# Optimization experiments

Measured on AMD Instinct MI355X. Metric: run time of the kernel, lower is better.

Reference implementation:

```python
import jax, jax.numpy as jnp
import numpy as np

B, D, N, H = 16384, 8, 64, 128   # batch, input_path_dim, cde_state_dim, vf_hidden_dim
NSIG = D + D * (D - 1) // 2       # Lyndon words up to depth 2: letters + pairs i<j


def setup_inputs() -> dict:
    key = jax.random.key(0)
    ks = jax.random.split(key, 6)
    g = lambda k, shape, scale: jax.random.normal(k, shape, jnp.float32) * scale
    return {
        "h": jax.random.normal(ks[0], (B, N), jnp.float32),
        "primitive_signature": jax.random.normal(ks[1], (B, NSIG), jnp.float32) * 0.1,
        "W1": g(ks[2], (H, N), (1.0 / N) ** 0.5),
        "b1": jnp.zeros((H,), jnp.float32),
        "W2": g(ks[3], (H, H), (1.0 / H) ** 0.5),
        "b2": jnp.zeros((H,), jnp.float32),
        "W3": g(ks[4], (D * N, H), (1.0 / H) ** 0.5),
        "b3": jnp.zeros((D * N,), jnp.float32),
    }


def reference(h, primitive_signature, W1, b1, W2, b2, W3, b3):
    d, n = D, N
    iu, ju = np.triu_indices(d, k=1)  # level-2 Lyndon words ij with i<j, lex order

    def vf(hv):  # MLP vector field: (n,) -> (d, n), one field per input channel
        z = jax.nn.softplus(W1 @ hv + b1)
        z = jax.nn.softplus(W2 @ z + b2)
        return jnp.tanh(W3 @ z + b3).reshape(d, n)

    def single(hv, sig):
        V = vf(hv)  # (d, n) level-1 brackets (the vector fields themselves)
        # JVP of the whole stacked field in direction t: J_{V_j}(h) @ t for all j
        jvp_dir = lambda t: jax.jvp(vf, (hv,), (t,))[1]  # (d, n)
        JV = jax.vmap(jvp_dir)(V)                         # (i, j, n) = J_{V_j} V_i
        # Lie bracket [V_i, V_j](h) = J_{V_j} V_i - J_{V_i} V_j
        br2 = JV - jnp.swapaxes(JV, 0, 1)                 # (i, j, n)
        lyn2 = br2[iu, ju]                                # (d*(d-1)/2, n)
        # log-ODE contraction: sum_w logsig_w * bracket_w(h)
        return sig[:d] @ V + sig[d:] @ lyn2               # (n,)

    return jax.vmap(single)(h, primitive_signature)
```

## Files before the change

### kernel.cpp

```cpp
#include <hip/hip_runtime.h>
#include <hip/hip_bf16.h>

#define NEL 16384

#define W1B_OFF 0
#define W2B_OFF 8192
#define W3B_OFF 24576
#define WS_WEIGHTS 90112
#define S1_OFF  90112
#define S2_OFF  (S1_OFF + NEL*128)
#define V_OFF   (S2_OFF + NEL*128)
#define DZ2_OFF (V_OFF + NEL*512)

typedef __attribute__((ext_vector_type(8))) short bf16x8;
typedef __attribute__((ext_vector_type(4))) float f32x4;

__device__ __forceinline__ float bf2f(unsigned int u16) {
    unsigned int x = u16 << 16;
    float f; __builtin_memcpy(&f, &x, 4); return f;
}
__device__ __forceinline__ unsigned short f2bf(float f) {
    unsigned int x; __builtin_memcpy(&x, &f, 4);
    x = (x + 0x7FFFu + ((x >> 16) & 1u)) >> 16;
    return (unsigned short)x;
}
__device__ __forceinline__ void unpack8(uint4 q, float* f) {
    f[0] = bf2f(q.x & 0xFFFFu); f[1] = bf2f(q.x >> 16);
    f[2] = bf2f(q.y & 0xFFFFu); f[3] = bf2f(q.y >> 16);
    f[4] = bf2f(q.z & 0xFFFFu); f[5] = bf2f(q.z >> 16);
    f[6] = bf2f(q.w & 0xFFFFu); f[7] = bf2f(q.w >> 16);
}
__device__ __forceinline__ void sp_sig(float x, float& sp, float& sig) {
    float t = __expf(-fabsf(x));
    float r = __builtin_amdgcn_rcpf(1.f + t);
    sig = (x >= 0.f) ? r : 1.f - r;
    sp  = fmaxf(x, 0.f) + __logf(1.f + t);
}
__device__ __forceinline__ float tanh_fast(float x) {
    float t = __expf(-2.f * fabsf(x));
    float y = (1.f - t) * __builtin_amdgcn_rcpf(1.f + t);
    unsigned int xb, yb;
    __builtin_memcpy(&xb, &x, 4);
    __builtin_memcpy(&yb, &y, 4);
    yb |= (xb & 0x80000000u);
    float rr; __builtin_memcpy(&rr, &yb, 4);
    return rr;
}
__device__ __forceinline__ bf16x8 ldfrag(const unsigned short* p) {
    return *reinterpret_cast<const bf16x8*>(p);
}
__device__ __forceinline__ void cpu4(unsigned short* dst, const unsigned short* src) {
    *reinterpret_cast<uint4*>(dst) = *reinterpret_cast<const uint4*>(src);
}

__global__ void prep_weights(const float* __restrict__ W1,
                             const float* __restrict__ W2,
                             const float* __restrict__ W3,
                             unsigned short* __restrict__ wb) {
    int i = blockIdx.x * blockDim.x + threadIdx.x;
    if (i >= WS_WEIGHTS) return;
    float v;
    if (i < W2B_OFF) v = W1[i];
    else if (i < W3B_OFF) v = W2[i - W2B_OFF];
    else v = W3[i - W3B_OFF];
    wb[i] = f2bf(v);
}

#define K12_LDS 39168
__global__ __launch_bounds__(256, 4)
void k12_fwd(const float* __restrict__ hg,
             const float* __restrict__ b1,
             const float* __restrict__ b2,
             const float* __restrict__ b3,
             unsigned short* __restrict__ wsb) {
    __shared__ __align__(16) char sm[K12_LDS];
    unsigned short* w1s = (unsigned short*)(sm);
    unsigned short* hs  = (unsigned short*)(sm + 18432);
    unsigned short* w2s = (unsigned short*)(sm);
    unsigned short* wc  = (unsigned short*)(sm);
    unsigned short* z1s = (unsigned short*)(sm + 34816);
    unsigned short* z2s = (unsigned short*)(sm + 34816);
    unsigned short* S1g = wsb + S1_OFF;
    unsigned short* S2g = wsb + S2_OFF;
    unsigned short* Vg  = wsb + V_OFF;

    const int tid = threadIdx.x;
    const int e0 = blockIdx.x * 16;
    const int lane = tid & 63;
    const int w = tid >> 6;
    const int r16 = lane & 15;
    const int kb = lane >> 4;
    const int crow = kb * 4;

    #pragma unroll
    for (int q = 0; q < 4; ++q) {
        int idx = q * 256 + tid;
        int row = idx >> 3, u4 = idx & 7;
        cpu4(&w1s[row * 72 + u4 * 8], &wsb[W1B_OFF + row * 64 + u4 * 8]);
    }
    {
        int row = tid >> 4, f4 = tid & 15;
        float4 hv = *reinterpret_cast<const float4*>(&hg[(e0 + row) * 64 + f4 * 4]);
        ushort2 lo = { f2bf(hv.x), f2bf(hv.y) };
        ushort2 hi = { f2bf(hv.z), f2bf(hv.w) };
        *reinterpret_cast<ushort2*>(&hs[row * 72 + f4 * 4]) = lo;
        *reinterpret_cast<ushort2*>(&hs[row * 72 + f4 * 4 + 2]) = hi;
    }
    __syncthreads();

    {
        const unsigned short* Ab = hs + r16 * 72 + kb * 8;
        bf16x8 a0 = ldfrag(Ab), a1 = ldfrag(Ab + 32);
        f32x4 acc[2] = {};
        #pragma unroll
        for (int t = 0; t < 2; ++t) {
            int col16 = (w * 2 + t) * 16 + r16;
            const unsigned short* Bb = w1s + col16 * 72 + kb * 8;
            acc[t] = __builtin_amdgcn_mfma_f32_16x16x32_bf16(a0, ldfrag(Bb), acc[t], 0, 0, 0);
            acc[t] = __builtin_amdgcn_mfma_f32_16x16x32_bf16(a1, ldfrag(Bb + 32), acc[t], 0, 0, 0);
        }
        #pragma unroll
        for (int t = 0; t < 2; ++t) {
            int col = (w * 2 + t) * 16 + r16;
            float bb = b1[col];
            #pragma unroll
            for (int rr = 0; rr < 4; ++rr) {
                int e = crow + rr;
                float sp, sg;
                sp_sig(acc[t][rr] + bb, sp, sg);
                z1s[e * 136 + col] = f2bf(sp);
                S1g[(e0 + e) * 128 + col] = f2bf(sg);
            }
        }
    }
    __syncthreads();

    #pragma unroll
    for (int q = 0; q < 8; ++q) {
        int idx = q * 256 + tid;
        int row = idx >> 4, u4 = idx & 15;
        cpu4(&w2s[row * 136 + u4 * 8], &wsb[W2B_OFF + row * 128 + u4 * 8]);
    }
    __syncthreads();

    {
        const unsigned short* Ab = z1s + r16 * 136 + kb * 8;
        bf16x8 a[4];
        #pragma unroll
        for (int ks = 0; ks < 4; ++ks) a[ks] = ldfrag(Ab + ks * 32);
        __syncthreads();
        f32x4 acc[2] = {};
        #pragma unroll
        for (int t = 0; t < 2; ++t) {
            int col16 = (w * 2 + t) * 16 + r16;
            const unsigned short* Bb = w2s + col16 * 136 + kb * 8;
            #pragma unroll
            for (int ks = 0; ks < 4; ++ks)
                acc[t] = __builtin_amdgcn_mfma_f32_16x16x32_bf16(a[ks], ldfrag(Bb + ks * 32), acc[t], 0, 0, 0);
        }
        #pragma unroll
        for (int t = 0; t < 2; ++t) {
            int col = (w * 2 + t) * 16 + r16;
            float bb = b2[col];
            #pragma unroll
            for (int rr = 0; rr < 4; ++rr) {
                int e = crow + rr;
                float sp, sg;
                sp_sig(acc[t][rr] + bb, sp, sg);
                z2s[e * 136 + col] = f2bf(sp);
                S2g[(e0 + e) * 128 + col] = f2bf(sg);
            }
        }
    }

    for (int nc = 0; nc < 4; ++nc) {
        __syncthreads();
        #pragma unroll
        for (int q = 0; q < 8; ++q) {
            int idx = q * 256 + tid;
            int row = idx >> 4, u4 = idx & 15;
            cpu4(&wc[row * 136 + u4 * 8], &wsb[W3B_OFF + (nc * 128 + row) * 128 + u4 * 8]);
        }
        __syncthreads();

        const unsigned short* Ab = z2s + r16 * 136 + kb * 8;
        bf16x8 a[4];
        #pragma unroll
        for (int ks = 0; ks < 4; ++ks) a[ks] = ldfrag(Ab + ks * 32);
        f32x4 acc[2] = {};
        #pragma unroll
        for (int t = 0; t < 2; ++t) {
            int col16 = (w * 2 + t) * 16 + r16;
            const unsigned short* Bb = wc + col16 * 136 + kb * 8;
            #pragma unroll
            for (int ks = 0; ks < 4; ++ks)
                acc[t] = __builtin_amdgcn_mfma_f32_16x16x32_bf16(a[ks], ldfrag(Bb + ks * 32), acc[t], 0, 0, 0);
        }
        #pragma unroll
        for (int t = 0; t < 2; ++t) {
            int c = nc * 128 + (w * 2 + t) * 16 + r16;
            float bb = b3[c];
            #pragma unroll
            for (int rr = 0; rr < 4; ++rr) {
                int e = crow + rr;
                float v = tanh_fast(acc[t][rr] + bb);
                Vg[(e0 + e) * 512 + c] = f2bf(v);
            }
        }
    }
}

#define K3_LDS 53376
__global__ __launch_bounds__(256, 3)
void k3_jvp12(const float* __restrict__ sigg,
              unsigned short* __restrict__ wsb) {
    __shared__ __align__(16) char sm[K3_LDS];
    unsigned short* vs   = (unsigned short*)(sm);
    unsigned short* w1s  = (unsigned short*)(sm + 8320);
    unsigned short* ts   = (unsigned short*)(sm + 26752);
    unsigned short* dz1s = (unsigned short*)(sm);
    unsigned short* w2s  = (unsigned short*)(sm + 17408);
    float* sigsm = (float*)(sm + 52224);
    const unsigned short* S1g = wsb + S1_OFF;
    const unsigned short* S2g = wsb + S2_OFF;
    const unsigned short* Vg  = wsb + V_OFF;
    unsigned short* DZ2g = wsb + DZ2_OFF;

    const int tid = threadIdx.x;
    const int e0 = blockIdx.x * 8;
    const int lane = tid & 63;
    const int w = tid >> 6;
    const int r16 = lane & 15;
    const int kb = lane >> 4;

    #pragma unroll
    for (int q = 0; q < 2; ++q) {
        int idx = q * 256 + tid;
        int row = idx >> 6, u4 = idx & 63;
        cpu4(&vs[row * 520 + u4 * 8], &Vg[(e0 + row) * 512 + u4 * 8]);
    }
    #pragma unroll
    for (int q = 0; q < 4; ++q) {
        int idx = q * 256 + tid;
        int row = idx >> 3, u4 = idx & 7;
        cpu4(&w1s[row * 72 + u4 * 8], &wsb[W1B_OFF + row * 64 + u4 * 8]);
    }
    #pragma unroll
    for (int q = 0; q < 2; ++q) {
        int idx = q * 256 + tid;
        if (idx < 288) sigsm[idx] = sigg[e0 * 36 + idx];
    }
    __syncthreads();

    {
        int m = tid >> 2, kq = tid & 3;
        int e = m >> 3, j = m & 7;
        float c8[8];
        #pragma unroll
        for (int i = 0; i < 8; ++i) {
            float v = 0.f;
            if (i < j) {
                int p = 7 * i - i * (i - 1) / 2 + (j - i - 1);
                v = sigsm[e * 36 + 8 + p];
            } else if (i > j) {
                int p = 7 * j - j * (j - 1) / 2 + (i - j - 1);
                v = -sigsm[e * 36 + 8 + p];
            }
            c8[i] = v;
        }
        float acc[16] = {};
        #pragma unroll
        for (int i = 0; i < 8; ++i) {
            uint4 qa = *reinterpret_cast<const uint4*>(&vs[e * 520 + i * 64 + kq * 16]);
            uint4 qb = *reinterpret_cast<const uint4*>(&vs[e * 520 + i * 64 + kq * 16 + 8]);
            float fa[8], fb[8];
            unpack8(qa, fa); unpack8(qb, fb);
            #pragma unroll
            for (int kk = 0; kk < 8; ++kk) {
                acc[kk]     += c8[i] * fa[kk];
                acc[kk + 8] += c8[i] * fb[kk];
            }
        }
        unsigned short o[16];
        #pragma unroll
        for (int kk = 0; kk < 16; ++kk) o[kk] = f2bf(acc[kk]);
        uint4 qo;
        qo.x = (unsigned int)o[0] | ((unsigned int)o[1] << 16);
        qo.y = (unsigned int)o[2] | ((unsigned int)o[3] << 16);
        qo.z = (unsigned int)o[4] | ((unsigned int)o[5] << 16);
        qo.w = (unsigned int)o[6] | ((unsigned int)o[7] << 16);
        *reinterpret_cast<uint4*>(&ts[m * 72 + kq * 16]) = qo;
        qo.x = (unsigned int)o[8]  | ((unsigned int)o[9]  << 16);
        qo.y = (unsigned int)o[10] | ((unsigned int)o[11] << 16);
        qo.z = (unsigned int)o[12] | ((unsigned int)o[13] << 16);
        qo.w = (unsigned int)o[14] | ((unsigned int)o[15] << 16);
        *reinterpret_cast<uint4*>(&ts[m * 72 + kq * 16 + 8]) = qo;
    }
    __syncthreads();

    float dz1v[8][4];
    const int rbase = w * 16 + kb * 4;
    const int e_loc = rbase >> 3;
    {
        const unsigned short* Ab = ts + (w * 16 + r16) * 72 + kb * 8;
        bf16x8 a0 = ldfrag(Ab), a1 = ldfrag(Ab + 32);
        f32x4 acc[8] = {};
        #pragma unroll
        for (int nt = 0; nt < 8; ++nt) {
            const unsigned short* Bb = w1s + (nt * 16 + r16) * 72 + kb * 8;
            acc[nt] = __builtin_amdgcn_mfma_f32_16x16x32_bf16(a0, ldfrag(Bb), acc[nt], 0, 0, 0);
            acc[nt] = __builtin_amdgcn_mfma_f32_16x16x32_bf16(a1, ldfrag(Bb + 32), acc[nt], 0, 0, 0);
        }
        #pragma unroll
        for (int nt = 0; nt < 8; ++nt) {
            int col = nt * 16 + r16;
            float s1v = bf2f(S1g[(e0 + e_loc) * 128 + col]);
            #pragma unroll
            for (int rr = 0; rr < 4; ++rr)
                dz1v[nt][rr] = acc[nt][rr] * s1v;
        }
    }
    __syncthreads();

    #pragma unroll
    for (int nt = 0; nt < 8; ++nt) {
        int col = nt * 16 + r16;
        #pragma unroll
        for (int rr = 0; rr < 4; ++rr)
            dz1s[(rbase + rr) * 136 + col] = f2bf(dz1v[nt][rr]);
    }
    #pragma unroll
    for (int q = 0; q < 8; ++q) {
        int idx = q * 256 + tid;
        int row = idx >> 4, u4 = idx & 15;
        cpu4(&w2s[row * 136 + u4 * 8], &wsb[W2B_OFF + row * 128 + u4 * 8]);
    }
    __syncthreads();

    {
        const unsigned short* Ab = dz1s + (w * 16 + r16) * 136 + kb * 8;
        bf16x8 a[4];
        #pragma unroll
        for (int ks = 0; ks < 4; ++ks) a[ks] = ldfrag(Ab + ks * 32);
        f32x4 acc[8] = {};
        #pragma unroll
        for (int nt = 0; nt < 8; ++nt) {
            const unsigned short* Bb = w2s + (nt * 16 + r16) * 136 + kb * 8;
            #pragma unroll
            for (int ks = 0; ks < 4; ++ks)
                acc[nt] = __builtin_amdgcn_mfma_f32_16x16x32_bf16(a[ks], ldfrag(Bb + ks * 32), acc[nt], 0, 0, 0);
        }
        #pragma unroll
        for (int nt = 0; nt < 8; ++nt) {
            int col = nt * 16 + r16;
            float s2v = bf2f(S2g[(e0 + e_loc) * 128 + col]);
            #pragma unroll
            for (int rr = 0; rr < 4; ++rr)
                DZ2g[(e0 * 8 + rbase + rr) * 128 + col] = f2bf(acc[nt][rr] * s2v);
        }
    }
}

#define K4_LDS 35392
__global__ __launch_bounds__(256, 4)
void k4_jvp3(const float* __restrict__ sigg,
             const unsigned short* __restrict__ wsb,
             float* __restrict__ out) {
    __shared__ __align__(16) char sm[K4_LDS];
    unsigned short* w3j0 = (unsigned short*)(sm);
    unsigned short* w3j1 = (unsigned short*)(sm + 17408);
    float*          sg1  = (float*)(sm + 34816);
    const unsigned short* Vg = wsb + V_OFF;
    const unsigned short* DZ2g = wsb + DZ2_OFF;

    const int tid = threadIdx.x;
    const int e0 = blockIdx.x * 16;
    const int lane = tid & 63;
    const int w = tid >> 6;
    const int r16 = lane & 15;
    const int kb = lane >> 4;
    const int crow = kb * 4;
    const int np = w * 16 + r16;

    if (tid < 128) {
        int e = tid >> 3, j7 = tid & 7;
        sg1[e * 9 + j7] = sigg[(e0 + e) * 36 + j7];
    }
    #pragma unroll
    for (int q = 0; q < 4; ++q) {
        int idx = q * 256 + tid;
        int row = idx >> 4, u4 = idx & 15;
        cpu4(&w3j0[row * 136 + u4 * 8], &wsb[W3B_OFF + row * 128 + u4 * 8]);
    }
    __syncthreads();

    float oacc[4] = {};
    const unsigned short* Agbase = DZ2g + (e0 + r16) * 8 * 128 + kb * 8;

    for (int j = 0; j < 8; ++j) {
        unsigned short* cur = (j & 1) ? w3j1 : w3j0;
        unsigned short* nxt = (j & 1) ? w3j0 : w3j1;
        if (j < 7) {
            #pragma unroll
            for (int q = 0; q < 4; ++q) {
                int idx = q * 256 + tid;
                int row = idx >> 4, u4 = idx & 15;
                cpu4(&nxt[row * 136 + u4 * 8], &wsb[W3B_OFF + ((j + 1) * 64 + row) * 128 + u4 * 8]);
            }
        }
        const unsigned short* Ag = Agbase + j * 128;
        bf16x8 a[4];
        #pragma unroll
        for (int ks = 0; ks < 4; ++ks) a[ks] = ldfrag(Ag + ks * 32);
        f32x4 acc = {};
        const unsigned short* Bb = cur + np * 136 + kb * 8;
        #pragma unroll
        for (int ks = 0; ks < 4; ++ks)
            acc = __builtin_amdgcn_mfma_f32_16x16x32_bf16(a[ks], ldfrag(Bb + ks * 32), acc, 0, 0, 0);

        #pragma unroll
        for (int rr = 0; rr < 4; ++rr) {
            int e = crow + rr;
            float v = bf2f(Vg[(e0 + e) * 512 + j * 64 + np]);
            float sv = sg1[e * 9 + j];
            oacc[rr] += sv * v + (1.f - v * v) * acc[rr];
        }
        __syncthreads();
    }

    #pragma unroll
    for (int rr = 0; rr < 4; ++rr)
        out[(e0 + crow + rr) * 64 + np] = oacc[rr];
}

extern "C" void kernel_launch(void* const* d_in, const int* in_sizes, int n_in,
                              void* d_out, int out_size, void* d_ws, size_t ws_size,
                              hipStream_t stream) {
    const float* hg  = (const float*)d_in[0];
    const float* sg  = (const float*)d_in[1];
    const float* W1  = (const float*)d_in[2];
    const float* b1  = (const float*)d_in[3];
    const float* W2  = (const float*)d_in[4];
    const float* b2  = (const float*)d_in[5];
    const float* W3  = (const float*)d_in[6];
    const float* b3  = (const float*)d_in[7];
    float* outp = (float*)d_out;
    unsigned short* wsb = (unsigned short*)d_ws;

    hipLaunchKernelGGL(prep_weights, dim3((WS_WEIGHTS + 255) / 256), dim3(256), 0, stream,
                       W1, W2, W3, wsb);
    hipLaunchKernelGGL(k12_fwd, dim3(NEL / 16), dim3(256), 0, stream, hg, b1, b2, b3, wsb);
    hipLaunchKernelGGL(k3_jvp12, dim3(NEL / 8), dim3(256), 0, stream, sg, wsb);
    hipLaunchKernelGGL(k4_jvp3, dim3(NEL / 16), dim3(256), 0, stream, sg, wsb, outp);
}
```

Baseline: 76.29 us.

## Read MFMA weight fragments directly from global memory instead of staging in LDS

In the forward kernel and the final JVP kernel, weight tiles are no longer copied into shared memory. Each lane loads its B fragments straight from global/L2, so the LDS copy loops and most block barriers go away, and shared memory per block shrinks sharply. The aim is to drop staging overhead and synchronisation and to raise occupancy. The cost is redundant global loads of the same weights across waves and blocks, plus uncoalesced row-strided fragment reads. Passing the workspace as separate const input and output pointers with __restrict__ is technically aliasing, since both point to the same buffer.

```diff
diff --git a/kernel.cpp b/kernel.cpp
--- a/kernel.cpp
+++ b/kernel.cpp
@@ -66,23 +66,21 @@
     wb[i] = f2bf(v);
 }
 
-#define K12_LDS 39168
+#define K12_LDS 11008
 __global__ __launch_bounds__(256, 4)
 void k12_fwd(const float* __restrict__ hg,
              const float* __restrict__ b1,
              const float* __restrict__ b2,
              const float* __restrict__ b3,
-             unsigned short* __restrict__ wsb) {
+             const unsigned short* __restrict__ wsb,
+             unsigned short* __restrict__ wso) {
     __shared__ __align__(16) char sm[K12_LDS];
-    unsigned short* w1s = (unsigned short*)(sm);
-    unsigned short* hs  = (unsigned short*)(sm + 18432);
-    unsigned short* w2s = (unsigned short*)(sm);
-    unsigned short* wc  = (unsigned short*)(sm);
-    unsigned short* z1s = (unsigned short*)(sm + 34816);
-    unsigned short* z2s = (unsigned short*)(sm + 34816);
-    unsigned short* S1g = wsb + S1_OFF;
-    unsigned short* S2g = wsb + S2_OFF;
-    unsigned short* Vg  = wsb + V_OFF;
+    unsigned short* hs  = (unsigned short*)(sm);
+    unsigned short* z1s = (unsigned short*)(sm + 2304);
+    unsigned short* z2s = (unsigned short*)(sm + 6656);
+    unsigned short* S1g = wso + S1_OFF;
+    unsigned short* S2g = wso + S2_OFF;
+    unsigned short* Vg  = wso + V_OFF;
 
     const int tid = threadIdx.x;
     const int e0 = blockIdx.x * 16;
@@ -92,12 +90,6 @@
     const int kb = lane >> 4;
     const int crow = kb * 4;
 
-    #pragma unroll
-    for (int q = 0; q < 4; ++q) {
-        int idx = q * 256 + tid;
-        int row = idx >> 3, u4 = idx & 7;
-        cpu4(&w1s[row * 72 + u4 * 8], &wsb[W1B_OFF + row * 64 + u4 * 8]);
-    }
     {
         int row = tid >> 4, f4 = tid & 15;
         float4 hv = *reinterpret_cast<const float4*>(&hg[(e0 + row) * 64 + f4 * 4]);
@@ -115,7 +107,7 @@
         #pragma unroll
         for (int t = 0; t < 2; ++t) {
             int col16 = (w * 2 + t) * 16 + r16;
-            const unsigned short* Bb = w1s + col16 * 72 + kb * 8;
+            const unsigned short* Bb = wsb + W1B_OFF + col16 * 64 + kb * 8;
             acc[t] = __builtin_amdgcn_mfma_f32_16x16x32_bf16(a0, ldfrag(Bb), acc[t], 0, 0, 0);
             acc[t] = __builtin_amdgcn_mfma_f32_16x16x32_bf16(a1, ldfrag(Bb + 32), acc[t], 0, 0, 0);
         }
@@ -135,25 +127,16 @@
     }
     __syncthreads();
 
-    #pragma unroll
-    for (int q = 0; q < 8; ++q) {
-        int idx = q * 256 + tid;
-        int row = idx >> 4, u4 = idx & 15;
-        cpu4(&w2s[row * 136 + u4 * 8], &wsb[W2B_OFF + row * 128 + u4 * 8]);
-    }
-    __syncthreads();
-
     {
         const unsigned short* Ab = z1s + r16 * 136 + kb * 8;
         bf16x8 a[4];
         #pragma unroll
         for (int ks = 0; ks < 4; ++ks) a[ks] = ldfrag(Ab + ks * 32);
-        __syncthreads();
         f32x4 acc[2] = {};
         #pragma unroll
         for (int t = 0; t < 2; ++t) {
             int col16 = (w * 2 + t) * 16 + r16;
-            const unsigned short* Bb = w2s + col16 * 136 + kb * 8;
+            const unsigned short* Bb = wsb + W2B_OFF + col16 * 128 + kb * 8;
             #pragma unroll
             for (int ks = 0; ks < 4; ++ks)
                 acc[t] = __builtin_amdgcn_mfma_f32_16x16x32_bf16(a[ks], ldfrag(Bb + ks * 32), acc[t], 0, 0, 0);
@@ -172,39 +155,30 @@
             }
         }
     }
-
-    for (int nc = 0; nc < 4; ++nc) {
-        __syncthreads();
-        #pragma unroll
-        for (int q = 0; q < 8; ++q) {
-            int idx = q * 256 + tid;
-            int row = idx >> 4, u4 = idx & 15;
-            cpu4(&wc[row * 136 + u4 * 8], &wsb[W3B_OFF + (nc * 128 + row) * 128 + u4 * 8]);
-        }
-        __syncthreads();
-
+    __syncthreads();
+
+    {
         const unsigned short* Ab = z2s + r16 * 136 + kb * 8;
         bf16x8 a[4];
         #pragma unroll
         for (int ks = 0; ks < 4; ++ks) a[ks] = ldfrag(Ab + ks * 32);
-        f32x4 acc[2] = {};
-        #pragma unroll
-        for (int t = 0; t < 2; ++t) {
-            int col16 = (w * 2 + t) * 16 + r16;
-            const unsigned short* Bb = wc + col16 * 136 + kb * 8;
-            #pragma unroll
-            for (int ks = 0; ks < 4; ++ks)
-                acc[t] = __builtin_amdgcn_mfma_f32_16x16x32_bf16(a[ks], ldfrag(Bb + ks * 32), acc[t], 0, 0, 0);
-        }
-        #pragma unroll
-        for (int t = 0; t < 2; ++t) {
-            int c = nc * 128 + (w * 2 + t) * 16 + r16;
-            float bb = b3[c];
-            #pragma unroll
-            for (int rr = 0; rr < 4; ++rr) {
-                int e = crow + rr;
-                float v = tanh_fast(acc[t][rr] + bb);
-                Vg[(e0 + e) * 512 + c] = f2bf(v);
+        #pragma unroll
+        for (int nc = 0; nc < 4; ++nc) {
+            #pragma unroll
+            for (int t = 0; t < 2; ++t) {
+                int c = nc * 128 + (w * 2 + t) * 16 + r16;
+                const unsigned short* Bb = wsb + W3B_OFF + c * 128 + kb * 8;
+                f32x4 acc = {};
+                #pragma unroll
+                for (int ks = 0; ks < 4; ++ks)
+                    acc = __builtin_amdgcn_mfma_f32_16x16x32_bf16(a[ks], ldfrag(Bb + ks * 32), acc, 0, 0, 0);
+                float bb = b3[c];
+                #pragma unroll
+                for (int rr = 0; rr < 4; ++rr) {
+                    int e = crow + rr;
+                    float v = tanh_fast(acc[rr] + bb);
+                    Vg[(e0 + e) * 512 + c] = f2bf(v);
+                }
             }
         }
     }
@@ -361,15 +335,11 @@
     }
 }
 
-#define K4_LDS 35392
 __global__ __launch_bounds__(256, 4)
 void k4_jvp3(const float* __restrict__ sigg,
              const unsigned short* __restrict__ wsb,
              float* __restrict__ out) {
-    __shared__ __align__(16) char sm[K4_LDS];
-    unsigned short* w3j0 = (unsigned short*)(sm);
-    unsigned short* w3j1 = (unsigned short*)(sm + 17408);
-    float*          sg1  = (float*)(sm + 34816);
+    __shared__ float sg1[16 * 9];
     const unsigned short* Vg = wsb + V_OFF;
     const unsigned short* DZ2g = wsb + DZ2_OFF;
 
@@ -386,37 +356,23 @@
         int e = tid >> 3, j7 = tid & 7;
         sg1[e * 9 + j7] = sigg[(e0 + e) * 36 + j7];
     }
-    #pragma unroll
-    for (int q = 0; q < 4; ++q) {
-        int idx = q * 256 + tid;
-        int row = idx >> 4, u4 = idx & 15;
-        cpu4(&w3j0[row * 136 + u4 * 8], &wsb[W3B_OFF + row * 128 + u4 * 8]);
-    }
     __syncthreads();
 
     float oacc[4] = {};
     const unsigned short* Agbase = DZ2g + (e0 + r16) * 8 * 128 + kb * 8;
-
+    const unsigned short* Bgbase = wsb + W3B_OFF + np * 128 + kb * 8;
+
+    #pragma unroll
     for (int j = 0; j < 8; ++j) {
-        unsigned short* cur = (j & 1) ? w3j1 : w3j0;
-        unsigned short* nxt = (j & 1) ? w3j0 : w3j1;
-        if (j < 7) {
-            #pragma unroll
-            for (int q = 0; q < 4; ++q) {
-                int idx = q * 256 + tid;
-                int row = idx >> 4, u4 = idx & 15;
-                cpu4(&nxt[row * 136 + u4 * 8], &wsb[W3B_OFF + ((j + 1) * 64 + row) * 128 + u4 * 8]);
-            }
-        }
         const unsigned short* Ag = Agbase + j * 128;
         bf16x8 a[4];
         #pragma unroll
         for (int ks = 0; ks < 4; ++ks) a[ks] = ldfrag(Ag + ks * 32);
+        const unsigned short* Bg = Bgbase + j * 64 * 128;
         f32x4 acc = {};
-        const unsigned short* Bb = cur + np * 136 + kb * 8;
         #pragma unroll
         for (int ks = 0; ks < 4; ++ks)
-            acc = __builtin_amdgcn_mfma_f32_16x16x32_bf16(a[ks], ldfrag(Bb + ks * 32), acc, 0, 0, 0);
+            acc = __builtin_amdgcn_mfma_f32_16x16x32_bf16(a[ks], ldfrag(Bg + ks * 32), acc, 0, 0, 0);
 
         #pragma unroll
         for (int rr = 0; rr < 4; ++rr) {
@@ -425,7 +381,6 @@
             float sv = sg1[e * 9 + j];
             oacc[rr] += sv * v + (1.f - v * v) * acc[rr];
         }
-        __syncthreads();
     }
 
     #pragma unroll
@@ -449,7 +404,7 @@
 
     hipLaunchKernelGGL(prep_weights, dim3((WS_WEIGHTS + 255) / 256), dim3(256), 0, stream,
                        W1, W2, W3, wsb);
-    hipLaunchKernelGGL(k12_fwd, dim3(NEL / 16), dim3(256), 0, stream, hg, b1, b2, b3, wsb);
+    hipLaunchKernelGGL(k12_fwd, dim3(NEL / 16), dim3(256), 0, stream, hg, b1, b2, b3, wsb, wsb);
     hipLaunchKernelGGL(k3_jvp12, dim3(NEL / 8), dim3(256), 0, stream, sg, wsb);
     hipLaunchKernelGGL(k4_jvp3, dim3(NEL / 16), dim3(256), 0, stream, sg, wsb, outp);
 }
```

New measurement: 92.99 us. 1.22x slower.

## Fuse JVP layer-3 kernel into layer-1/2 kernel, keeping DZ2 in LDS

Applied to the files above, without the earlier changes.

Merges the k4 JVP-layer-3 kernel into k3, so the DZ2 intermediate stays in shared memory and never round-trips through global memory, and one launch is removed. The row mapping is changed to j-major so each 16-row MFMA tile holds two j values. Each wave computes both halves and keeps only its own, and partial sums are then combined through LDS. S1/S2 scale rows are staged into LDS. The costs are redundant MFMA work in the layer-3 stage (half the lanes discard results), a larger LDS footprint, and W3 being reloaded per 8-element block instead of per 16.

```diff
diff --git a/kernel.cpp b/kernel.cpp
--- a/kernel.cpp
+++ b/kernel.cpp
@@ -10,7 +10,6 @@
 #define S1_OFF  90112
 #define S2_OFF  (S1_OFF + NEL*128)
 #define V_OFF   (S2_OFF + NEL*128)
-#define DZ2_OFF (V_OFF + NEL*512)
 
 typedef __attribute__((ext_vector_type(8))) short bf16x8;
 typedef __attribute__((ext_vector_type(4))) float f32x4;
@@ -210,21 +209,30 @@
     }
 }
 
-#define K3_LDS 53376
+#define C3_SLOT 52224
+#define C3_LDS  54272
 __global__ __launch_bounds__(256, 3)
-void k3_jvp12(const float* __restrict__ sigg,
-              unsigned short* __restrict__ wsb) {
-    __shared__ __align__(16) char sm[K3_LDS];
-    unsigned short* vs   = (unsigned short*)(sm);
-    unsigned short* w1s  = (unsigned short*)(sm + 8320);
-    unsigned short* ts   = (unsigned short*)(sm + 26752);
-    unsigned short* dz1s = (unsigned short*)(sm);
-    unsigned short* w2s  = (unsigned short*)(sm + 17408);
-    float* sigsm = (float*)(sm + 52224);
+void k3_all(const float* __restrict__ sigg,
+            const unsigned short* __restrict__ wsb,
+            float* __restrict__ out) {
+    __shared__ __align__(16) char sm[C3_LDS];
+    unsigned short* vs    = (unsigned short*)(sm);
+    unsigned short* w1s   = (unsigned short*)(sm + 8320);
+    unsigned short* ts    = (unsigned short*)(sm + 26752);
+    float*          sigsm = (float*)(sm + 35968);
+    unsigned short* dz1s  = (unsigned short*)(sm);
+    unsigned short* w2s   = (unsigned short*)(sm + 17408);
+    unsigned short* dz2s  = (unsigned short*)(sm);
+    unsigned short* w3j0  = (unsigned short*)(sm + 17408);
+    unsigned short* w3j1  = (unsigned short*)(sm + 34816);
+    unsigned short* s1s   = (unsigned short*)(sm + C3_SLOT);
+    unsigned short* s2s   = (unsigned short*)(sm + C3_SLOT);
+    float*          sig1f = (float*)(sm + C3_SLOT);
+    float*          pjf   = (float*)(sm + C3_SLOT);
+
     const unsigned short* S1g = wsb + S1_OFF;
     const unsigned short* S2g = wsb + S2_OFF;
     const unsigned short* Vg  = wsb + V_OFF;
-    unsigned short* DZ2g = wsb + DZ2_OFF;
 
     const int tid = threadIdx.x;
     const int e0 = blockIdx.x * 8;
@@ -232,6 +240,7 @@
     const int w = tid >> 6;
     const int r16 = lane & 15;
     const int kb = lane >> 4;
+    const int crow = kb * 4;
 
     #pragma unroll
     for (int q = 0; q < 2; ++q) {
@@ -250,11 +259,15 @@
         int idx = q * 256 + tid;
         if (idx < 288) sigsm[idx] = sigg[e0 * 36 + idx];
     }
+    if (tid < 128) {
+        int row = tid >> 4, u4 = tid & 15;
+        cpu4(&s1s[row * 128 + u4 * 8], &S1g[(e0 + row) * 128 + u4 * 8]);
+    }
     __syncthreads();
 
     {
         int m = tid >> 2, kq = tid & 3;
-        int e = m >> 3, j = m & 7;
+        int j = m >> 3, e = m & 7;
         float c8[8];
         #pragma unroll
         for (int i = 0; i < 8; ++i) {
@@ -298,9 +311,12 @@
     }
     __syncthreads();
 
+    const int rbase = w * 16 + crow;
+    int e4[4];
+    #pragma unroll
+    for (int rr = 0; rr < 4; ++rr) e4[rr] = (crow + rr) & 7;
+
     float dz1v[8][4];
-    const int rbase = w * 16 + kb * 4;
-    const int e_loc = rbase >> 3;
     {
         const unsigned short* Ab = ts + (w * 16 + r16) * 72 + kb * 8;
         bf16x8 a0 = ldfrag(Ab), a1 = ldfrag(Ab + 32);
@@ -314,10 +330,9 @@
         #pragma unroll
         for (int nt = 0; nt < 8; ++nt) {
             int col = nt * 16 + r16;
-            float s1v = bf2f(S1g[(e0 + e_loc) * 128 + col]);
             #pragma unroll
             for (int rr = 0; rr < 4; ++rr)
-                dz1v[nt][rr] = acc[nt][rr] * s1v;
+                dz1v[nt][rr] = acc[nt][rr] * bf2f(s1s[e4[rr] * 128 + col]);
         }
     }
     __syncthreads();
@@ -335,8 +350,13 @@
         int row = idx >> 4, u4 = idx & 15;
         cpu4(&w2s[row * 136 + u4 * 8], &wsb[W2B_OFF + row * 128 + u4 * 8]);
     }
-    __syncthreads();
-
+    if (tid < 128) {
+        int row = tid >> 4, u4 = tid & 15;
+        cpu4(&s2s[row * 128 + u4 * 8], &S2g[(e0 + row) * 128 + u4 * 8]);
+    }
+    __syncthreads();
+
+    float dz2v[8][4];
     {
         const unsigned short* Ab = dz1s + (w * 16 + r16) * 136 + kb * 8;
         bf16x8 a[4];
@@ -353,38 +373,19 @@
         #pragma unroll
         for (int nt = 0; nt < 8; ++nt) {
             int col = nt * 16 + r16;
-            float s2v = bf2f(S2g[(e0 + e_loc) * 128 + col]);
             #pragma unroll
             for (int rr = 0; rr < 4; ++rr)
-                DZ2g[(e0 * 8 + rbase + rr) * 128 + col] = f2bf(acc[nt][rr] * s2v);
-        }
-    }
-}
-
-#define K4_LDS 35392
-__global__ __launch_bounds__(256, 4)
-void k4_jvp3(const float* __restrict__ sigg,
-             const unsigned short* __restrict__ wsb,
-             float* __restrict__ out) {
-    __shared__ __align__(16) char sm[K4_LDS];
-    unsigned short* w3j0 = (unsigned short*)(sm);
-    unsigned short* w3j1 = (unsigned short*)(sm + 17408);
-    float*          sg1  = (float*)(sm + 34816);
-    const unsigned short* Vg = wsb + V_OFF;
-    const unsigned short* DZ2g = wsb + DZ2_OFF;
-
-    const int tid = threadIdx.x;
-    const int e0 = blockIdx.x * 16;
-    const int lane = tid & 63;
-    const int w = tid >> 6;
-    const int r16 = lane & 15;
-    const int kb = lane >> 4;
-    const int crow = kb * 4;
-    const int np = w * 16 + r16;
-
-    if (tid < 128) {
-        int e = tid >> 3, j7 = tid & 7;
-        sg1[e * 9 + j7] = sigg[(e0 + e) * 36 + j7];
+                dz2v[nt][rr] = acc[nt][rr] * bf2f(s2s[e4[rr] * 128 + col]);
+        }
+    }
+    __syncthreads();
+
+    #pragma unroll
+    for (int nt = 0; nt < 8; ++nt) {
+        int col = nt * 16 + r16;
+        #pragma unroll
+        for (int rr = 0; rr < 4; ++rr)
+            dz2s[(rbase + rr) * 136 + col] = f2bf(dz2v[nt][rr]);
     }
     #pragma unroll
     for (int q = 0; q < 4; ++q) {
@@ -392,11 +393,16 @@
         int row = idx >> 4, u4 = idx & 15;
         cpu4(&w3j0[row * 136 + u4 * 8], &wsb[W3B_OFF + row * 128 + u4 * 8]);
     }
-    __syncthreads();
-
+    if (tid < 64) {
+        sig1f[tid] = sigg[(e0 + (tid >> 3)) * 36 + (tid & 7)];
+    }
+    __syncthreads();
+
+    const int np = w * 16 + r16;
+    const int myhalf = kb >> 1;
     float oacc[4] = {};
-    const unsigned short* Agbase = DZ2g + (e0 + r16) * 8 * 128 + kb * 8;
-
+
+    #pragma unroll
     for (int j = 0; j < 8; ++j) {
         unsigned short* cur = (j & 1) ? w3j1 : w3j0;
         unsigned short* nxt = (j & 1) ? w3j0 : w3j1;
@@ -408,29 +414,42 @@
                 cpu4(&nxt[row * 136 + u4 * 8], &wsb[W3B_OFF + ((j + 1) * 64 + row) * 128 + u4 * 8]);
             }
         }
-        const unsigned short* Ag = Agbase + j * 128;
+        int mt = j >> 1;
+        const unsigned short* Ab = dz2s + (mt * 16 + r16) * 136 + kb * 8;
         bf16x8 a[4];
         #pragma unroll
-        for (int ks = 0; ks < 4; ++ks) a[ks] = ldfrag(Ag + ks * 32);
+        for (int ks = 0; ks < 4; ++ks) a[ks] = ldfrag(Ab + ks * 32);
+        const unsigned short* Bb = cur + np * 136 + kb * 8;
         f32x4 acc = {};
-        const unsigned short* Bb = cur + np * 136 + kb * 8;
         #pragma unroll
         for (int ks = 0; ks < 4; ++ks)
             acc = __builtin_amdgcn_mfma_f32_16x16x32_bf16(a[ks], ldfrag(Bb + ks * 32), acc, 0, 0, 0);
 
+        if (myhalf == (j & 1)) {
+            #pragma unroll
+            for (int rr = 0; rr < 4; ++rr) {
+                int e = (crow + rr) & 7;
+                float v = bf2f(Vg[(e0 + e) * 512 + j * 64 + np]);
+                float sv = sig1f[e * 8 + j];
+                oacc[rr] += sv * v + (1.f - v * v) * acc[rr];
+            }
+        }
+        __syncthreads();
+    }
+
+    if (kb < 2) {
+        #pragma unroll
+        for (int rr = 0; rr < 4; ++rr)
+            pjf[(crow + rr) * 64 + np] = oacc[rr];
+    }
+    __syncthreads();
+    if (kb >= 2) {
         #pragma unroll
         for (int rr = 0; rr < 4; ++rr) {
-            int e = crow + rr;
-            float v = bf2f(Vg[(e0 + e) * 512 + j * 64 + np]);
-            float sv = sg1[e * 9 + j];
-            oacc[rr] += sv * v + (1.f - v * v) * acc[rr];
-        }
-        __syncthreads();
-    }
-
-    #pragma unroll
-    for (int rr = 0; rr < 4; ++rr)
-        out[(e0 + crow + rr) * 64 + np] = oacc[rr];
+            int e = (crow - 8) + rr;
+            out[(e0 + e) * 64 + np] = pjf[e * 64 + np] + oacc[rr];
+        }
+    }
 }
 
 extern "C" void kernel_launch(void* const* d_in, const int* in_sizes, int n_in,
@@ -450,6 +469,5 @@
     hipLaunchKernelGGL(prep_weights, dim3((WS_WEIGHTS + 255) / 256), dim3(256), 0, stream,
                        W1, W2, W3, wsb);
     hipLaunchKernelGGL(k12_fwd, dim3(NEL / 16), dim3(256), 0, stream, hg, b1, b2, b3, wsb);
-    hipLaunchKernelGGL(k3_jvp12, dim3(NEL / 8), dim3(256), 0, stream, sg, wsb);
-    hipLaunchKernelGGL(k4_jvp3, dim3(NEL / 16), dim3(256), 0, stream, sg, wsb, outp);
-}
+    hipLaunchKernelGGL(k3_all, dim3(NEL / 8), dim3(256), 0, stream, sg, wsb, outp);
+}
```

After: 84.66 us. 11.0% more time.

## Shrink k3 LDS footprint to raise occupancy by streaming V and halving W2

Applied to the files above, without the earlier changes.

Kernel k3 no longer stages V rows in shared memory; the bracket contraction reads V straight from global memory. The second GEMM now loads W2 in two 64-row halves into a reused buffer, with an extra barrier between them. Together these cut LDS from about 53KB to 36KB, so launch bounds go from 3 to 4 blocks per CU to hide latency better. The cost is direct global loads for V and more synchronisation and load phases in the W2 stage.

```diff
diff --git a/kernel.cpp b/kernel.cpp
--- a/kernel.cpp
+++ b/kernel.cpp
@@ -210,17 +210,16 @@
     }
 }
 
-#define K3_LDS 53376
-__global__ __launch_bounds__(256, 3)
+#define K3_LDS 35968
+__global__ __launch_bounds__(256, 4)
 void k3_jvp12(const float* __restrict__ sigg,
               unsigned short* __restrict__ wsb) {
     __shared__ __align__(16) char sm[K3_LDS];
-    unsigned short* vs   = (unsigned short*)(sm);
-    unsigned short* w1s  = (unsigned short*)(sm + 8320);
-    unsigned short* ts   = (unsigned short*)(sm + 26752);
+    unsigned short* w1s  = (unsigned short*)(sm);
+    unsigned short* ts   = (unsigned short*)(sm + 18432);
+    float*          sigsm= (float*)(sm + 34816);
     unsigned short* dz1s = (unsigned short*)(sm);
-    unsigned short* w2s  = (unsigned short*)(sm + 17408);
-    float* sigsm = (float*)(sm + 52224);
+    unsigned short* w2sh = (unsigned short*)(sm + 17408);
     const unsigned short* S1g = wsb + S1_OFF;
     const unsigned short* S2g = wsb + S2_OFF;
     const unsigned short* Vg  = wsb + V_OFF;
@@ -233,12 +232,6 @@
     const int r16 = lane & 15;
     const int kb = lane >> 4;
 
-    #pragma unroll
-    for (int q = 0; q < 2; ++q) {
-        int idx = q * 256 + tid;
-        int row = idx >> 6, u4 = idx & 63;
-        cpu4(&vs[row * 520 + u4 * 8], &Vg[(e0 + row) * 512 + u4 * 8]);
-    }
     #pragma unroll
     for (int q = 0; q < 4; ++q) {
         int idx = q * 256 + tid;
@@ -268,11 +261,12 @@
             }
             c8[i] = v;
         }
+        const unsigned short* Vrow = &Vg[(e0 + e) * 512 + kq * 16];
         float acc[16] = {};
         #pragma unroll
         for (int i = 0; i < 8; ++i) {
-            uint4 qa = *reinterpret_cast<const uint4*>(&vs[e * 520 + i * 64 + kq * 16]);
-            uint4 qb = *reinterpret_cast<const uint4*>(&vs[e * 520 + i * 64 + kq * 16 + 8]);
+            uint4 qa = *reinterpret_cast<const uint4*>(Vrow + i * 64);
+            uint4 qb = *reinterpret_cast<const uint4*>(Vrow + i * 64 + 8);
             float fa[8], fb[8];
             unpack8(qa, fa); unpack8(qb, fb);
             #pragma unroll
@@ -330,29 +324,60 @@
             dz1s[(rbase + rr) * 136 + col] = f2bf(dz1v[nt][rr]);
     }
     #pragma unroll
-    for (int q = 0; q < 8; ++q) {
+    for (int q = 0; q < 4; ++q) {
         int idx = q * 256 + tid;
         int row = idx >> 4, u4 = idx & 15;
-        cpu4(&w2s[row * 136 + u4 * 8], &wsb[W2B_OFF + row * 128 + u4 * 8]);
-    }
-    __syncthreads();
-
+        cpu4(&w2sh[row * 136 + u4 * 8], &wsb[W2B_OFF + row * 128 + u4 * 8]);
+    }
+    __syncthreads();
+
+    bf16x8 a2[4];
     {
         const unsigned short* Ab = dz1s + (w * 16 + r16) * 136 + kb * 8;
-        bf16x8 a[4];
-        #pragma unroll
-        for (int ks = 0; ks < 4; ++ks) a[ks] = ldfrag(Ab + ks * 32);
-        f32x4 acc[8] = {};
-        #pragma unroll
-        for (int nt = 0; nt < 8; ++nt) {
-            const unsigned short* Bb = w2s + (nt * 16 + r16) * 136 + kb * 8;
+        #pragma unroll
+        for (int ks = 0; ks < 4; ++ks) a2[ks] = ldfrag(Ab + ks * 32);
+    }
+
+    {
+        f32x4 acc[4] = {};
+        #pragma unroll
+        for (int nt = 0; nt < 4; ++nt) {
+            const unsigned short* Bb = w2sh + (nt * 16 + r16) * 136 + kb * 8;
             #pragma unroll
             for (int ks = 0; ks < 4; ++ks)
-                acc[nt] = __builtin_amdgcn_mfma_f32_16x16x32_bf16(a[ks], ldfrag(Bb + ks * 32), acc[nt], 0, 0, 0);
-        }
-        #pragma unroll
-        for (int nt = 0; nt < 8; ++nt) {
+                acc[nt] = __builtin_amdgcn_mfma_f32_16x16x32_bf16(a2[ks], ldfrag(Bb + ks * 32), acc[nt], 0, 0, 0);
+        }
+        #pragma unroll
+        for (int nt = 0; nt < 4; ++nt) {
             int col = nt * 16 + r16;
+            float s2v = bf2f(S2g[(e0 + e_loc) * 128 + col]);
+            #pragma unroll
+            for (int rr = 0; rr < 4; ++rr)
+                DZ2g[(e0 * 8 + rbase + rr) * 128 + col] = f2bf(acc[nt][rr] * s2v);
+        }
+    }
+    __syncthreads();
+
+    #pragma unroll
+    for (int q = 0; q < 4; ++q) {
+        int idx = q * 256 + tid;
+        int row = idx >> 4, u4 = idx & 15;
+        cpu4(&w2sh[row * 136 + u4 * 8], &wsb[W2B_OFF + (64 + row) * 128 + u4 * 8]);
+    }
+    __syncthreads();
+
+    {
+        f32x4 acc[4] = {};
+        #pragma unroll
+        for (int nt = 0; nt < 4; ++nt) {
+            const unsigned short* Bb = w2sh + (nt * 16 + r16) * 136 + kb * 8;
+            #pragma unroll
+            for (int ks = 0; ks < 4; ++ks)
+                acc[nt] = __builtin_amdgcn_mfma_f32_16x16x32_bf16(a2[ks], ldfrag(Bb + ks * 32), acc[nt], 0, 0, 0);
+        }
+        #pragma unroll
+        for (int nt = 0; nt < 4; ++nt) {
+            int col = 64 + nt * 16 + r16;
             float s2v = bf2f(S2g[(e0 + e_loc) * 128 + col]);
             #pragma unroll
             for (int rr = 0; rr < 4; ++rr)
```

New measurement: 73.57 us. 3.6% less time.
